# Kernel optimization log

Measured on AMD Instinct MI355X. Metric: run time of the kernel, lower is better.

Reference implementation:

```python
import jax, jax.numpy as jnp
import numpy as np
from jax import lax

L, B, T, C, F = 4, 4, 2048, 1024, 4096  # n_layer, batch, ctx_len, n_embd(=dim_att), dim_ffn
EPS = 1e-5


def setup_inputs() -> dict:
    key = jax.random.key(0)
    ks = jax.random.split(key, 16)
    s = 0.02
    d = {}
    d["x"] = jax.random.normal(ks[0], (B, T, C), jnp.float32)
    d["ln0_w"] = jnp.ones((C,), jnp.float32)
    d["ln0_b"] = jnp.zeros((C,), jnp.float32)
    d["ln1_w"] = jnp.ones((L, C), jnp.float32)
    d["ln1_b"] = jnp.zeros((L, C), jnp.float32)
    d["ln2_w"] = jnp.ones((L, C), jnp.float32)
    d["ln2_b"] = jnp.zeros((L, C), jnp.float32)
    d["time_decay"] = jax.random.normal(ks[1], (L, C), jnp.float32) * 0.5
    d["time_first"] = jax.random.normal(ks[2], (L, C), jnp.float32) * 0.5 + jnp.float32(np.log(0.3))
    d["tmk"] = jax.random.uniform(ks[3], (L, C), jnp.float32)
    d["tmv"] = jax.random.uniform(ks[4], (L, C), jnp.float32)
    d["tmr"] = jax.random.uniform(ks[5], (L, C), jnp.float32)
    d["Wk"] = jax.random.normal(ks[6], (L, C, C), jnp.float32) * s
    d["Wv"] = jax.random.normal(ks[7], (L, C, C), jnp.float32) * s
    d["Wr"] = jax.random.normal(ks[8], (L, C, C), jnp.float32) * s
    d["Wo"] = jax.random.normal(ks[9], (L, C, C), jnp.float32) * s
    d["cmk"] = jax.random.uniform(ks[10], (L, C), jnp.float32)
    d["cmr"] = jax.random.uniform(ks[11], (L, C), jnp.float32)
    d["Wck"] = jax.random.normal(ks[12], (L, F, C), jnp.float32) * s  # key: n_embd -> dim_ffn
    d["Wcv"] = jax.random.normal(ks[13], (L, C, F), jnp.float32) * s  # value: dim_ffn -> n_embd
    d["Wcr"] = jax.random.normal(ks[14], (L, C, C), jnp.float32) * s  # receptance
    return d


def layernorm(x, w, b):
    m = jnp.mean(x, axis=-1, keepdims=True)
    v = jnp.var(x, axis=-1, keepdims=True)
    return (x - m) * lax.rsqrt(v + EPS) * w + b


def time_shift(x):
    # ZeroPad2d((0,0,1,-1)): shift sequence right by one, zero at t=0
    return jnp.pad(x, ((0, 0), (1, 0), (0, 0)))[:, :-1]


def wkv(time_decay, time_first, k, v):
    # numerically-stable RWKV-4 WKV recurrence; k,v: [B,T,C]
    w = -jnp.exp(time_decay)  # [C]
    u = time_first            # [C]
    kt = jnp.swapaxes(k, 0, 1)  # [T,B,C]
    vt = jnp.swapaxes(v, 0, 1)
    Bn, Cn = k.shape[0], k.shape[2]
    init = (jnp.zeros((Bn, Cn), k.dtype), jnp.zeros((Bn, Cn), k.dtype),
            jnp.full((Bn, Cn), -1e38, k.dtype))

    def step(carry, kv):
        aa, bb, pp = carry
        kk, vv = kv
        ww = u + kk
        qq = jnp.maximum(pp, ww)
        e1 = jnp.exp(pp - qq)
        e2 = jnp.exp(ww - qq)
        out = (e1 * aa + e2 * vv) / (e1 * bb + e2)
        ww2 = pp + w
        qq2 = jnp.maximum(ww2, kk)
        e1b = jnp.exp(ww2 - qq2)
        e2b = jnp.exp(kk - qq2)
        return (e1b * aa + e2b * vv, e1b * bb + e2b, qq2), out

    _, out = lax.scan(step, init, (kt, vt))
    return jnp.swapaxes(out, 0, 1)  # [B,T,C]


def reference(x, ln0_w, ln0_b, ln1_w, ln1_b, ln2_w, ln2_b, time_decay, time_first,
              tmk, tmv, tmr, Wk, Wv, Wr, Wo, cmk, cmr, Wck, Wcv, Wcr):
    x = layernorm(x, ln0_w, ln0_b)  # ln0 on layer 0
    for l in range(L):
        # --- TimeMix ---
        h = layernorm(x, ln1_w[l], ln1_b[l])
        hh = time_shift(h)
        xk = h * tmk[l] + hh * (1 - tmk[l])
        xv = h * tmv[l] + hh * (1 - tmv[l])
        xr = h * tmr[l] + hh * (1 - tmr[l])
        k = jnp.einsum('btc,oc->bto', xk, Wk[l])
        v = jnp.einsum('btc,oc->bto', xv, Wv[l])
        sr = jax.nn.sigmoid(jnp.einsum('btc,oc->bto', xr, Wr[l]))
        rwkv = sr * wkv(time_decay[l], time_first[l], k, v)
        x = x + jnp.einsum('bto,co->btc', rwkv, Wo[l])
        # --- ChannelMix ---
        h = layernorm(x, ln2_w[l], ln2_b[l])
        hh = time_shift(h)
        xk = h * cmk[l] + hh * (1 - cmk[l])
        xr = h * cmr[l] + hh * (1 - cmr[l])
        kf = jnp.einsum('btc,fc->btf', xk, Wck[l])
        kf = jnp.square(jax.nn.relu(kf))
        kv = jnp.einsum('btf,cf->btc', kf, Wcv[l])
        x = x + jax.nn.sigmoid(jnp.einsum('btc,oc->bto', xr, Wcr[l])) * kv
    return x
```

## Files before the change

### kernel.cpp

```cpp
#include <hip/hip_runtime.h>
#include <cstdint>

#define TT 2048
#define CCH 1024
#define FFD 4096
#define EPSV 1e-5f
#define NCHK 32
#define CHKL 64

typedef __attribute__((ext_vector_type(4))) float floatx4;
typedef __attribute__((ext_vector_type(8))) short shortx8;

__device__ __forceinline__ unsigned short f32_to_bf16(float f){
  union { float f; unsigned int u; } x; x.f = f;
  unsigned int r = x.u + 0x7fffu + ((x.u >> 16) & 1u);
  return (unsigned short)(r >> 16);
}
__device__ __forceinline__ float bf16_to_f32(unsigned short h){
  union { unsigned int u; float f; } x; x.u = ((unsigned int)h) << 16;
  return x.f;
}
__device__ __forceinline__ float wave_sum(float v){
  #pragma unroll
  for (int o = 32; o > 0; o >>= 1) v += __shfl_down(v, o, 64);
  return v;
}
__device__ __forceinline__ void async16(const void* g, void* l){
  __builtin_amdgcn_global_load_lds((const __attribute__((address_space(1))) void*)g,
                                   (__attribute__((address_space(3))) void*)l, 16, 0, 0);
}

struct CvtArgs {
  const float* s[7];
  unsigned short* d[7];
  int n4[7];
};
__global__ __launch_bounds__(256) void cvt7_kernel(CvtArgs a){
  const int seg = blockIdx.y;
  const float* __restrict__ s = a.s[seg];
  unsigned short* __restrict__ d = a.d[seg];
  const int n4 = a.n4[seg];
  for (int i = blockIdx.x * 256 + threadIdx.x; i < n4; i += gridDim.x * 256) {
    float4 v = ((const float4*)s)[i];
    union { unsigned short u[4]; uint2 p; } o;
    o.u[0] = f32_to_bf16(v.x); o.u[1] = f32_to_bf16(v.y);
    o.u[2] = f32_to_bf16(v.z); o.u[3] = f32_to_bf16(v.w);
    *(uint2*)&d[(long)i * 4] = o.p;
  }
}

__global__ __launch_bounds__(256) void ln0_kernel(const float* __restrict__ xin,
    const float* __restrict__ w, const float* __restrict__ b, float* __restrict__ xo){
  const int row = blockIdx.x, tid = threadIdx.x;
  const float* xr = xin + (long)row * CCH;
  float c4[4]; float s = 0.f, s2 = 0.f;
  #pragma unroll
  for (int j = 0; j < 4; j++){ c4[j] = xr[tid + j*256]; s += c4[j]; s2 += c4[j]*c4[j]; }
  s = wave_sum(s); s2 = wave_sum(s2);
  __shared__ float red[2][4];
  const int wid = tid >> 6, lane = tid & 63;
  if (lane == 0){ red[0][wid] = s; red[1][wid] = s2; }
  __syncthreads();
  const float S  = red[0][0]+red[0][1]+red[0][2]+red[0][3];
  const float S2 = red[1][0]+red[1][1]+red[1][2]+red[1][3];
  const float inv = 1.f / CCH;
  const float m = S * inv;
  const float rs = rsqrtf(S2 * inv - m*m + EPSV);
  float* xout = xo + (long)row * CCH;
  #pragma unroll
  for (int j = 0; j < 4; j++){ int c = tid + j*256; xout[c] = (c4[j]-m)*rs*w[c] + b[c]; }
}

template<int NOUT>
__global__ __launch_bounds__(256) void ln_mix(
    const float* __restrict__ x,
    const float* __restrict__ lw, const float* __restrict__ lb,
    const float* __restrict__ mk, const float* __restrict__ mv, const float* __restrict__ mr,
    unsigned short* __restrict__ xk, unsigned short* __restrict__ xv, unsigned short* __restrict__ xr)
{
  const int row = blockIdx.x;
  const int t = row & (TT - 1);
  const int tid = threadIdx.x;
  const float* xc = x + (long)row * CCH;
  const float* xp = xc - CCH;
  float c4[4], p4[4];
  float s1=0.f, s2=0.f, s3=0.f, s4=0.f;
  #pragma unroll
  for (int j = 0; j < 4; j++){
    const int c = tid + j*256;
    c4[j] = xc[c];
    p4[j] = (t > 0) ? xp[c] : 0.f;
    s1 += c4[j]; s2 += c4[j]*c4[j];
    s3 += p4[j]; s4 += p4[j]*p4[j];
  }
  s1 = wave_sum(s1); s2 = wave_sum(s2); s3 = wave_sum(s3); s4 = wave_sum(s4);
  __shared__ float red[4][4];
  const int wid = tid >> 6, lane = tid & 63;
  if (lane == 0){ red[wid][0]=s1; red[wid][1]=s2; red[wid][2]=s3; red[wid][3]=s4; }
  __syncthreads();
  const float S1 = red[0][0]+red[1][0]+red[2][0]+red[3][0];
  const float S2 = red[0][1]+red[1][1]+red[2][1]+red[3][1];
  const float S3 = red[0][2]+red[1][2]+red[2][2]+red[3][2];
  const float S4 = red[0][3]+red[1][3]+red[2][3]+red[3][3];
  const float inv = 1.f / CCH;
  const float m1 = S1*inv; const float r1 = rsqrtf(S2*inv - m1*m1 + EPSV);
  const float m0 = S3*inv; const float r0 = rsqrtf(S4*inv - m0*m0 + EPSV);
  #pragma unroll
  for (int j = 0; j < 4; j++){
    const int c = tid + j*256;
    const long o = (long)row * CCH + c;
    const float wv = lw[c], bv = lb[c];
    const float h  = (c4[j]-m1)*r1*wv + bv;
    const float hp = (t > 0) ? ((p4[j]-m0)*r0*wv + bv) : 0.f;
    const float a = mk[c]; xk[o] = f32_to_bf16(h*a + hp*(1.f-a));
    if (NOUT == 3){ const float q = mv[c]; xv[o] = f32_to_bf16(h*q + hp*(1.f-q)); }
    const float g = mr[c]; xr[o] = f32_to_bf16(h*g + hp*(1.f-g));
  }
}

__global__ __launch_bounds__(256) void wkv_pass1(
    const unsigned short* __restrict__ kin, const unsigned short* __restrict__ vin,
    const float* __restrict__ td,
    float* __restrict__ sta, float* __restrict__ stb, float* __restrict__ stp)
{
  const int c = blockIdx.x * 256 + threadIdx.x;
  const int chunk = blockIdx.y, b = blockIdx.z;
  const float w = -__expf(td[c]);
  const long base = ((long)b * TT + (long)chunk * CHKL) * CCH + c;
  float aa = 0.f, bb = 0.f, pp = -1e38f;
  for (int t0 = 0; t0 < CHKL; t0 += 8) {
    float kr[8], vr[8];
    #pragma unroll
    for (int j = 0; j < 8; j++){
      const long o = base + (long)(t0 + j) * CCH;
      kr[j] = bf16_to_f32(kin[o]);
      vr[j] = bf16_to_f32(vin[o]);
    }
    #pragma unroll
    for (int j = 0; j < 8; j++){
      const float kk = kr[j], vv = vr[j];
      const float ww2 = pp + w;
      const float qq2 = fmaxf(ww2, kk);
      const float e1b = __expf(ww2 - qq2), e2b = __expf(kk - qq2);
      aa = e1b*aa + e2b*vv; bb = e1b*bb + e2b; pp = qq2;
    }
  }
  const long si = (long)chunk * 4096 + b * CCH + c;
  sta[si] = aa; stb[si] = bb; stp[si] = pp;
}

__global__ __launch_bounds__(256) void wkv_combine(
    const float* __restrict__ td,
    const float* __restrict__ sta, const float* __restrict__ stb, const float* __restrict__ stp,
    float* __restrict__ ina, float* __restrict__ inb, float* __restrict__ inp)
{
  const int idx = blockIdx.x * 256 + threadIdx.x;
  const int c = idx & (CCH - 1);
  const float wn = -__expf(td[c]) * (float)CHKL;
  float a = 0.f, b = 0.f, p = -1e38f;
  for (int j0 = 0; j0 < NCHK; j0 += 8) {
    float la[8], lb[8], lp[8];
    #pragma unroll
    for (int j = 0; j < 8; j++){
      const long si = (long)(j0 + j) * 4096 + idx;
      la[j] = sta[si]; lb[j] = stb[si]; lp[j] = stp[si];
    }
    #pragma unroll
    for (int j = 0; j < 8; j++){
      const long si = (long)(j0 + j) * 4096 + idx;
      ina[si] = a; inb[si] = b; inp[si] = p;
      const float pd = p + wn;
      const float q = fmaxf(pd, lp[j]);
      const float e1 = __expf(pd - q), e2 = __expf(lp[j] - q);
      a = e1*a + e2*la[j]; b = e1*b + e2*lb[j]; p = q;
    }
  }
}

__global__ __launch_bounds__(256) void wkv_pass2(
    const unsigned short* __restrict__ kin, const unsigned short* __restrict__ vin,
    const unsigned short* __restrict__ srin,
    const float* __restrict__ td, const float* __restrict__ tf,
    const float* __restrict__ ina, const float* __restrict__ inb, const float* __restrict__ inp,
    unsigned short* __restrict__ out)
{
  const int c = blockIdx.x * 256 + threadIdx.x;
  const int chunk = blockIdx.y, b = blockIdx.z;
  const float w = -__expf(td[c]);
  const float u = tf[c];
  const long si = (long)chunk * 4096 + b * CCH + c;
  float aa = ina[si], bb = inb[si], pp = inp[si];
  const long base = ((long)b * TT + (long)chunk * CHKL) * CCH + c;
  for (int t0 = 0; t0 < CHKL; t0 += 8) {
    float kr[8], vr[8], sr[8];
    #pragma unroll
    for (int j = 0; j < 8; j++){
      const long o = base + (long)(t0 + j) * CCH;
      kr[j] = bf16_to_f32(kin[o]);
      vr[j] = bf16_to_f32(vin[o]);
      sr[j] = bf16_to_f32(srin[o]);
    }
    #pragma unroll
    for (int j = 0; j < 8; j++){
      const float kk = kr[j], vv = vr[j];
      const float ww = u + kk;
      const float qq = fmaxf(pp, ww);
      const float e1 = __expf(pp - qq), e2 = __expf(ww - qq);
      const float outv = (e1*aa + e2*vv) / (e1*bb + e2);
      const float ww2 = pp + w;
      const float qq2 = fmaxf(ww2, kk);
      const float e1b = __expf(ww2 - qq2), e2b = __expf(kk - qq2);
      aa = e1b*aa + e2b*vv; bb = e1b*bb + e2b; pp = qq2;
      out[base + (long)(t0 + j) * CCH] = f32_to_bf16(sr[j] * outv);
    }
  }
}

#define BK 64

enum { EP_BF16 = 0, EP_ADD = 3, EP_MULADD = 4, EP_KVR = 5, EP_FFN1 = 6 };

template<int EPI, int BMt>
__global__ __launch_bounds__(256, 3) void gemm_bt(
    const unsigned short* __restrict__ A,
    const unsigned short* __restrict__ W,
    int N, const int K,
    unsigned short* __restrict__ outb,
    float* __restrict__ xres,
    const unsigned short* __restrict__ rr,
    const unsigned short* __restrict__ A2,
    const unsigned short* __restrict__ W2,
    unsigned short* __restrict__ outb2,
    const int N2)
{
  constexpr int MR = BMt / 2 / 16;
  constexpr int NR = 4;
  constexpr int AI = BMt / 32;

  const int bm = blockIdx.x;
  int bn = blockIdx.y;
  bool sig = false;
  if (EPI == EP_KVR) {
    const long z = blockIdx.z;
    const long Mfull = (long)gridDim.x * BMt;
    A    += z * Mfull * K;
    W    += z * (long)N * K;
    outb += z * Mfull * N;
    sig = (blockIdx.z == 2);
  }
  if (EPI == EP_FFN1) {
    if (blockIdx.z == 1) {
      if (bn >= N2 / 128) return;
      A = A2; W = W2; outb = outb2; N = N2; sig = true;
    }
  }
  __shared__ unsigned short lA[BMt * BK];
  __shared__ unsigned short lW[128 * BK];
  const int tid = threadIdx.x;
  const int wid = tid >> 6, lane = tid & 63;
  const int wm = (wid >> 1), wn = (wid & 1);
  const int quad = lane >> 4, r16 = lane & 15;

  const int srow = tid >> 3;
  const int scol = (tid & 7) ^ (srow & 7);
  const unsigned short* Ag = A + ((long)(bm * BMt + srow)) * K + scol * 8;
  const unsigned short* Wg = W + ((long)(bn * 128 + srow)) * K + scol * 8;
  const long rs32 = (long)32 * K;

  const int sw0 = ((quad)     ^ (r16 & 7)) * 8;
  const int sw1 = ((4 + quad) ^ (r16 & 7)) * 8;

  const floatx4 zf = {0.f, 0.f, 0.f, 0.f};
  floatx4 acc[MR][NR];
  #pragma unroll
  for (int i = 0; i < MR; i++)
    #pragma unroll
    for (int j = 0; j < NR; j++) acc[i][j] = zf;

  for (int k0 = 0; k0 < K; k0 += BK) {
    __syncthreads();
    #pragma unroll
    for (int i = 0; i < 4; i++) {
      if (BMt == 256) {
        async16(Ag + (long)(2*i)   * rs32 + k0, &lA[((2*i)   * 256 + tid) * 8]);
        async16(Ag + (long)(2*i+1) * rs32 + k0, &lA[((2*i+1) * 256 + tid) * 8]);
      } else {
        async16(Ag + (long)i * rs32 + k0, &lA[(i * 256 + tid) * 8]);
      }
      async16(Wg + (long)i * rs32 + k0, &lW[(i * 256 + tid) * 8]);
    }
    __syncthreads();
    #pragma unroll
    for (int kk = 0; kk < 2; kk++) {
      const int sw = kk ? sw1 : sw0;
      shortx8 af[MR], bf[NR];
      #pragma unroll
      for (int m = 0; m < MR; m++)
        af[m] = *(const shortx8*)&lA[(wm * (MR*16) + m*16 + r16) * 64 + sw];
      #pragma unroll
      for (int n = 0; n < NR; n++)
        bf[n] = *(const shortx8*)&lW[(wn * 64 + n*16 + r16) * 64 + sw];
      #pragma unroll
      for (int m = 0; m < MR; m++)
        #pragma unroll
        for (int n = 0; n < NR; n++)
          acc[m][n] = __builtin_amdgcn_mfma_f32_16x16x32_bf16(af[m], bf[n], acc[m][n], 0, 0, 0);
    }
  }

  const int colBase = bn * 128 + wn * 64 + r16;
  #pragma unroll
  for (int m = 0; m < MR; m++) {
    const int rowBase = bm * BMt + wm * (MR*16) + m * 16 + quad * 4;
    #pragma unroll
    for (int n = 0; n < NR; n++) {
      const int col = colBase + n * 16;
      #pragma unroll
      for (int r = 0; r < 4; r++) {
        const long idx = (long)(rowBase + r) * N + col;
        const float val = acc[m][n][r];
        if (EPI == EP_KVR)       outb[idx] = sig ? f32_to_bf16(1.f / (1.f + __expf(-val)))
                                                 : f32_to_bf16(val);
        else if (EPI == EP_FFN1) {
          if (sig) outb[idx] = f32_to_bf16(1.f / (1.f + __expf(-val)));
          else     { const float t = val > 0.f ? val : 0.f; outb[idx] = f32_to_bf16(t * t); }
        }
        else if (EPI == EP_ADD)  xres[idx] += val;
        else if (EPI == EP_MULADD) xres[idx] = fmaf(bf16_to_f32(rr[idx]), val, xres[idx]);
        else                     outb[idx] = f32_to_bf16(val);
      }
    }
  }
}

extern "C" void kernel_launch(void* const* d_in, const int* in_sizes, int n_in,
                              void* d_out, int out_size, void* d_ws, size_t ws_size,
                              hipStream_t stream)
{
  const float* x_in       = (const float*)d_in[0];
  const float* ln0_w      = (const float*)d_in[1];
  const float* ln0_b      = (const float*)d_in[2];
  const float* ln1_w      = (const float*)d_in[3];
  const float* ln1_b      = (const float*)d_in[4];
  const float* ln2_w      = (const float*)d_in[5];
  const float* ln2_b      = (const float*)d_in[6];
  const float* time_decay = (const float*)d_in[7];
  const float* time_first = (const float*)d_in[8];
  const float* tmk        = (const float*)d_in[9];
  const float* tmv        = (const float*)d_in[10];
  const float* tmr        = (const float*)d_in[11];
  const float* Wk         = (const float*)d_in[12];
  const float* Wv         = (const float*)d_in[13];
  const float* Wr         = (const float*)d_in[14];
  const float* Wo         = (const float*)d_in[15];
  const float* cmk        = (const float*)d_in[16];
  const float* cmr        = (const float*)d_in[17];
  const float* Wck        = (const float*)d_in[18];
  const float* Wcv        = (const float*)d_in[19];
  const float* Wcr        = (const float*)d_in[20];
  float* x = (float*)d_out;

  const int M = 4 * TT;
  const long lCC = (long)CCH * CCH;
  const long lFC = (long)FFD * CCH;
  const long MC  = (long)M * CCH;

  unsigned short* wsl  = (unsigned short*)d_ws;
  unsigned short* wkb  = wsl;
  unsigned short* wvb  = wkb + lCC;
  unsigned short* wrb  = wvb + lCC;
  unsigned short* wob  = wrb + lCC;
  unsigned short* wcrb = wob + lCC;
  unsigned short* wckb = wcrb + lCC;
  unsigned short* wcvb = wckb + lFC;
  unsigned short* xk   = wcvb + lFC;
  unsigned short* xv   = xk + MC;
  unsigned short* xr   = xv + MC;
  unsigned short* kbuf = xr + MC;
  unsigned short* vbuf = kbuf + MC;
  unsigned short* sbuf = vbuf + MC;
  unsigned short* kfb  = kbuf;
  unsigned short* rrb  = kbuf + (long)M * FFD;

  float* sta = (float*)xk;
  float* stb = sta + (long)NCHK * 4096;
  float* stp = stb + (long)NCHK * 4096;
  float* ina = stp + (long)NCHK * 4096;
  float* inb = ina + (long)NCHK * 4096;
  float* inp = inb + (long)NCHK * 4096;

  ln0_kernel<<<M, 256, 0, stream>>>(x_in, ln0_w, ln0_b, x);

  const dim3 gkvr(M / 256, CCH / 128, 3);
  const dim3 g1  (M / 128, CCH / 128);
  const dim3 gffn(M / 256, FFD / 128, 2);
  const dim3 gw(CCH / 256, NCHK, 4);

  for (int l = 0; l < 4; l++) {
    CvtArgs ca;
    ca.s[0] = Wk  + (long)l * lCC; ca.d[0] = wkb;  ca.n4[0] = (int)(lCC / 4);
    ca.s[1] = Wv  + (long)l * lCC; ca.d[1] = wvb;  ca.n4[1] = (int)(lCC / 4);
    ca.s[2] = Wr  + (long)l * lCC; ca.d[2] = wrb;  ca.n4[2] = (int)(lCC / 4);
    ca.s[3] = Wo  + (long)l * lCC; ca.d[3] = wob;  ca.n4[3] = (int)(lCC / 4);
    ca.s[4] = Wcr + (long)l * lCC; ca.d[4] = wcrb; ca.n4[4] = (int)(lCC / 4);
    ca.s[5] = Wck + (long)l * lFC; ca.d[5] = wckb; ca.n4[5] = (int)(lFC / 4);
    ca.s[6] = Wcv + (long)l * lFC; ca.d[6] = wcvb; ca.n4[6] = (int)(lFC / 4);
    cvt7_kernel<<<dim3(512, 7), 256, 0, stream>>>(ca);

    const float* td_l = time_decay + l*CCH;
    const float* tf_l = time_first + l*CCH;

    ln_mix<3><<<M, 256, 0, stream>>>(x, ln1_w + l*CCH, ln1_b + l*CCH,
                                     tmk + l*CCH, tmv + l*CCH, tmr + l*CCH, xk, xv, xr);
    gemm_bt<EP_KVR, 256><<<gkvr, 256, 0, stream>>>(xk, wkb, CCH, CCH, kbuf, nullptr,
                                              nullptr, nullptr, nullptr, nullptr, 0);
    wkv_pass1 <<<gw, 256, 0, stream>>>(kbuf, vbuf, td_l, sta, stb, stp);
    wkv_combine<<<16, 256, 0, stream>>>(td_l, sta, stb, stp, ina, inb, inp);
    wkv_pass2 <<<gw, 256, 0, stream>>>(kbuf, vbuf, sbuf, td_l, tf_l, ina, inb, inp, xv);
    gemm_bt<EP_ADD, 128><<<g1, 256, 0, stream>>>(xv, wob, CCH, CCH, nullptr, x, nullptr,
                                             nullptr, nullptr, nullptr, 0);

    ln_mix<2><<<M, 256, 0, stream>>>(x, ln2_w + l*CCH, ln2_b + l*CCH,
                                     cmk + l*CCH, nullptr, cmr + l*CCH, xk, nullptr, xr);
    gemm_bt<EP_FFN1, 256><<<gffn, 256, 0, stream>>>(xk, wckb, FFD, CCH, kfb, nullptr,
                                               nullptr, xr, wcrb, rrb, CCH);
    gemm_bt<EP_MULADD, 128><<<g1, 256, 0, stream>>>(kfb, wcvb, CCH, FFD, nullptr, x, rrb,
                                               nullptr, nullptr, nullptr, 0);
  }
}
```

Measured before the change: 1.622 ms.

## Triple-buffer GEMM LDS tiles with async prefetch and BK=32

Replaces the single-buffered BK=64 GEMM main loop, which had two barriers per k-step, with a three-stage LDS ring of BK=32 tiles. Global-to-LDS async loads run two steps ahead, guarded by explicit vmcnt waits and one barrier per step. MFMA sections are raised in priority with setprio, and the swizzle is adapted to the narrower tile. This is meant to hide global load latency behind MFMA work. In exchange it takes more LDS and lowers the occupancy hint from 3 to 2 blocks per CU.

```diff
diff --git a/kernel.cpp b/kernel.cpp
--- a/kernel.cpp
+++ b/kernel.cpp
@@ -216,12 +216,12 @@
   }
 }
 
-#define BK 64
+#define BK 32
 
 enum { EP_BF16 = 0, EP_ADD = 3, EP_MULADD = 4, EP_KVR = 5, EP_FFN1 = 6 };
 
 template<int EPI, int BMt>
-__global__ __launch_bounds__(256, 3) void gemm_bt(
+__global__ __launch_bounds__(256, 2) void gemm_bt(
     const unsigned short* __restrict__ A,
     const unsigned short* __restrict__ W,
     int N, const int K,
@@ -235,7 +235,9 @@
 {
   constexpr int MR = BMt / 2 / 16;
   constexpr int NR = 4;
-  constexpr int AI = BMt / 32;
+  constexpr int LA = BMt * 4 / 256;
+  constexpr int LB = 2;
+  constexpr int LPT = LA + LB;
 
   const int bm = blockIdx.x;
   int bn = blockIdx.y;
@@ -254,21 +256,34 @@
       A = A2; W = W2; outb = outb2; N = N2; sig = true;
     }
   }
-  __shared__ unsigned short lA[BMt * BK];
-  __shared__ unsigned short lW[128 * BK];
+  __shared__ unsigned short lA[3][BMt * BK];
+  __shared__ unsigned short lW[3][128 * BK];
   const int tid = threadIdx.x;
   const int wid = tid >> 6, lane = tid & 63;
   const int wm = (wid >> 1), wn = (wid & 1);
   const int quad = lane >> 4, r16 = lane & 15;
-
-  const int srow = tid >> 3;
-  const int scol = (tid & 7) ^ (srow & 7);
-  const unsigned short* Ag = A + ((long)(bm * BMt + srow)) * K + scol * 8;
-  const unsigned short* Wg = W + ((long)(bn * 128 + srow)) * K + scol * 8;
-  const long rs32 = (long)32 * K;
-
-  const int sw0 = ((quad)     ^ (r16 & 7)) * 8;
-  const int sw1 = ((4 + quad) ^ (r16 & 7)) * 8;
+  const int WR = wm * (MR * 16);
+
+  const unsigned short* aSrc[LA]; int aDst[LA];
+  #pragma unroll
+  for (int i = 0; i < LA; i++) {
+    const int P = i * 256 + tid;
+    const int row = P >> 2;
+    const int c = (P & 3) ^ (row & 3);
+    aSrc[i] = A + (long)(bm * BMt + row) * K + c * 8;
+    aDst[i] = P * 8;
+  }
+  const unsigned short* bSrc[LB]; int bDst[LB];
+  #pragma unroll
+  for (int i = 0; i < LB; i++) {
+    const int P = i * 256 + tid;
+    const int row = P >> 2;
+    const int c = (P & 3) ^ (row & 3);
+    bSrc[i] = W + (long)(bn * 128 + row) * K + c * 8;
+    bDst[i] = P * 8;
+  }
+
+  const int swq = (quad ^ (r16 & 3)) * 8;
 
   const floatx4 zf = {0.f, 0.f, 0.f, 0.f};
   floatx4 acc[MR][NR];
@@ -277,41 +292,59 @@
     #pragma unroll
     for (int j = 0; j < NR; j++) acc[i][j] = zf;
 
-  for (int k0 = 0; k0 < K; k0 += BK) {
-    __syncthreads();
-    #pragma unroll
-    for (int i = 0; i < 4; i++) {
-      if (BMt == 256) {
-        async16(Ag + (long)(2*i)   * rs32 + k0, &lA[((2*i)   * 256 + tid) * 8]);
-        async16(Ag + (long)(2*i+1) * rs32 + k0, &lA[((2*i+1) * 256 + tid) * 8]);
-      } else {
-        async16(Ag + (long)i * rs32 + k0, &lA[(i * 256 + tid) * 8]);
-      }
-      async16(Wg + (long)i * rs32 + k0, &lW[(i * 256 + tid) * 8]);
-    }
-    __syncthreads();
-    #pragma unroll
-    for (int kk = 0; kk < 2; kk++) {
-      const int sw = kk ? sw1 : sw0;
-      shortx8 af[MR], bf[NR];
+  const int NT = K / BK;
+
+  #pragma unroll
+  for (int tt = 0; tt < 2; ++tt) {
+    const long ko = (long)tt * BK;
+    #pragma unroll
+    for (int i = 0; i < LA; i++) async16(aSrc[i] + ko, &lA[tt][aDst[i]]);
+    #pragma unroll
+    for (int i = 0; i < LB; i++) async16(bSrc[i] + ko, &lW[tt][bDst[i]]);
+  }
+  asm volatile("s_waitcnt vmcnt(%0)" :: "n"(LPT) : "memory");
+  __builtin_amdgcn_s_barrier();
+  __builtin_amdgcn_sched_barrier(0);
+
+  int s = 0, s2 = 2;
+  for (int t = 0; t < NT; ++t) {
+    if (t + 2 < NT) {
+      const long ko = (long)(t + 2) * BK;
       #pragma unroll
-      for (int m = 0; m < MR; m++)
-        af[m] = *(const shortx8*)&lA[(wm * (MR*16) + m*16 + r16) * 64 + sw];
+      for (int i = 0; i < LA; i++) async16(aSrc[i] + ko, &lA[s2][aDst[i]]);
+      #pragma unroll
+      for (int i = 0; i < LB; i++) async16(bSrc[i] + ko, &lW[s2][bDst[i]]);
+    }
+    shortx8 af[MR], bf[NR];
+    #pragma unroll
+    for (int m = 0; m < MR; m++)
+      af[m] = *(const shortx8*)&lA[s][(WR + m * 16 + r16) * BK + swq];
+    #pragma unroll
+    for (int n = 0; n < NR; n++)
+      bf[n] = *(const shortx8*)&lW[s][(wn * 64 + n * 16 + r16) * BK + swq];
+    __builtin_amdgcn_s_setprio(1);
+    #pragma unroll
+    for (int m = 0; m < MR; m++)
       #pragma unroll
       for (int n = 0; n < NR; n++)
-        bf[n] = *(const shortx8*)&lW[(wn * 64 + n*16 + r16) * 64 + sw];
-      #pragma unroll
-      for (int m = 0; m < MR; m++)
-        #pragma unroll
-        for (int n = 0; n < NR; n++)
-          acc[m][n] = __builtin_amdgcn_mfma_f32_16x16x32_bf16(af[m], bf[n], acc[m][n], 0, 0, 0);
-    }
+        acc[m][n] = __builtin_amdgcn_mfma_f32_16x16x32_bf16(af[m], bf[n], acc[m][n], 0, 0, 0);
+    __builtin_amdgcn_s_setprio(0);
+    __builtin_amdgcn_sched_barrier(0);
+    if (t + 2 < NT)      asm volatile("s_waitcnt vmcnt(%0)" :: "n"(LPT) : "memory");
+    else if (t + 1 < NT) asm volatile("s_waitcnt vmcnt(0)" ::: "memory");
+    if (t + 1 < NT) {
+      asm volatile("s_waitcnt lgkmcnt(0)" ::: "memory");
+      __builtin_amdgcn_s_barrier();
+      __builtin_amdgcn_sched_barrier(0);
+    }
+    s = (s == 2) ? 0 : s + 1;
+    s2 = (s2 == 2) ? 0 : s2 + 1;
   }
 
   const int colBase = bn * 128 + wn * 64 + r16;
   #pragma unroll
   for (int m = 0; m < MR; m++) {
-    const int rowBase = bm * BMt + wm * (MR*16) + m * 16 + quad * 4;
+    const int rowBase = bm * BMt + WR + m * 16 + quad * 4;
     #pragma unroll
     for (int n = 0; n < NR; n++) {
       const int col = colBase + n * 16;
```

Result: slower. 1.923 ms (+18.6%).

## Fuse weight conversion into ln_mix, inline WKV combine, add double-buffered GEMM

Applied to the files above, without the earlier changes.

The bf16 weight conversion now runs as extra grid rows of the first ln_mix launch, which removes one kernel launch per layer. The chunk-state combine kernel is removed: each pass2 block recomputes its prefix state serially over the earlier chunks, trading redundant work for one fewer launch and less buffer traffic. A new 128x128 double-buffered GEMM with async LDS loads and occupancy of two handles the output and FFN value projections. The risks are a slower GEMM and load imbalance from the prefix loop in later chunks.

```diff
diff --git a/kernel.cpp b/kernel.cpp
--- a/kernel.cpp
+++ b/kernel.cpp
@@ -35,8 +35,7 @@
   unsigned short* d[7];
   int n4[7];
 };
-__global__ __launch_bounds__(256) void cvt7_kernel(CvtArgs a){
-  const int seg = blockIdx.y;
+__device__ __forceinline__ void cvt_body(const CvtArgs& a, int seg){
   const float* __restrict__ s = a.s[seg];
   unsigned short* __restrict__ d = a.d[seg];
   const int n4 = a.n4[seg];
@@ -72,7 +71,7 @@
 }
 
 template<int NOUT>
-__global__ __launch_bounds__(256) void ln_mix(
+__device__ __forceinline__ void lnmix_body(
     const float* __restrict__ x,
     const float* __restrict__ lw, const float* __restrict__ lb,
     const float* __restrict__ mk, const float* __restrict__ mv, const float* __restrict__ mr,
@@ -118,6 +117,29 @@
   }
 }
 
+template<int NOUT>
+__global__ __launch_bounds__(256) void ln_mix(
+    const float* __restrict__ x,
+    const float* __restrict__ lw, const float* __restrict__ lb,
+    const float* __restrict__ mk, const float* __restrict__ mv, const float* __restrict__ mr,
+    unsigned short* __restrict__ xk, unsigned short* __restrict__ xv, unsigned short* __restrict__ xr)
+{
+  lnmix_body<NOUT>(x, lw, lb, mk, mv, mr, xk, xv, xr);
+}
+
+__global__ __launch_bounds__(256) void lnmix3_cvt(CvtArgs a,
+    const float* __restrict__ x,
+    const float* __restrict__ lw, const float* __restrict__ lb,
+    const float* __restrict__ mk, const float* __restrict__ mv, const float* __restrict__ mr,
+    unsigned short* __restrict__ xk, unsigned short* __restrict__ xv, unsigned short* __restrict__ xr)
+{
+  if (blockIdx.y == 0) {
+    lnmix_body<3>(x, lw, lb, mk, mv, mr, xk, xv, xr);
+  } else {
+    cvt_body(a, blockIdx.y - 1);
+  }
+}
+
 __global__ __launch_bounds__(256) void wkv_pass1(
     const unsigned short* __restrict__ kin, const unsigned short* __restrict__ vin,
     const float* __restrict__ td,
@@ -149,47 +171,27 @@
   sta[si] = aa; stb[si] = bb; stp[si] = pp;
 }
 
-__global__ __launch_bounds__(256) void wkv_combine(
-    const float* __restrict__ td,
-    const float* __restrict__ sta, const float* __restrict__ stb, const float* __restrict__ stp,
-    float* __restrict__ ina, float* __restrict__ inb, float* __restrict__ inp)
-{
-  const int idx = blockIdx.x * 256 + threadIdx.x;
-  const int c = idx & (CCH - 1);
-  const float wn = -__expf(td[c]) * (float)CHKL;
-  float a = 0.f, b = 0.f, p = -1e38f;
-  for (int j0 = 0; j0 < NCHK; j0 += 8) {
-    float la[8], lb[8], lp[8];
-    #pragma unroll
-    for (int j = 0; j < 8; j++){
-      const long si = (long)(j0 + j) * 4096 + idx;
-      la[j] = sta[si]; lb[j] = stb[si]; lp[j] = stp[si];
-    }
-    #pragma unroll
-    for (int j = 0; j < 8; j++){
-      const long si = (long)(j0 + j) * 4096 + idx;
-      ina[si] = a; inb[si] = b; inp[si] = p;
-      const float pd = p + wn;
-      const float q = fmaxf(pd, lp[j]);
-      const float e1 = __expf(pd - q), e2 = __expf(lp[j] - q);
-      a = e1*a + e2*la[j]; b = e1*b + e2*lb[j]; p = q;
-    }
-  }
-}
-
 __global__ __launch_bounds__(256) void wkv_pass2(
     const unsigned short* __restrict__ kin, const unsigned short* __restrict__ vin,
     const unsigned short* __restrict__ srin,
     const float* __restrict__ td, const float* __restrict__ tf,
-    const float* __restrict__ ina, const float* __restrict__ inb, const float* __restrict__ inp,
+    const float* __restrict__ sta, const float* __restrict__ stb, const float* __restrict__ stp,
     unsigned short* __restrict__ out)
 {
   const int c = blockIdx.x * 256 + threadIdx.x;
   const int chunk = blockIdx.y, b = blockIdx.z;
   const float w = -__expf(td[c]);
   const float u = tf[c];
-  const long si = (long)chunk * 4096 + b * CCH + c;
-  float aa = ina[si], bb = inb[si], pp = inp[si];
+  const float wn = w * (float)CHKL;
+  float aa = 0.f, bb = 0.f, pp = -1e38f;
+  for (int j = 0; j < chunk; ++j) {
+    const long sj = (long)j * 4096 + b * CCH + c;
+    const float la = sta[sj], lb = stb[sj], lp = stp[sj];
+    const float pd = pp + wn;
+    const float q = fmaxf(pd, lp);
+    const float e1 = __expf(pd - q), e2 = __expf(lp - q);
+    aa = e1*aa + e2*la; bb = e1*bb + e2*lb; pp = q;
+  }
   const long base = ((long)b * TT + (long)chunk * CHKL) * CCH + c;
   for (int t0 = 0; t0 < CHKL; t0 += 8) {
     float kr[8], vr[8], sr[8];
@@ -235,7 +237,6 @@
 {
   constexpr int MR = BMt / 2 / 16;
   constexpr int NR = 4;
-  constexpr int AI = BMt / 32;
 
   const int bm = blockIdx.x;
   int bn = blockIdx.y;
@@ -328,6 +329,103 @@
         else if (EPI == EP_ADD)  xres[idx] += val;
         else if (EPI == EP_MULADD) xres[idx] = fmaf(bf16_to_f32(rr[idx]), val, xres[idx]);
         else                     outb[idx] = f32_to_bf16(val);
+      }
+    }
+  }
+}
+
+template<int EPI>
+__global__ __launch_bounds__(256, 2) void gemm2p(
+    const unsigned short* __restrict__ A,
+    const unsigned short* __restrict__ W,
+    const int N, const int K,
+    float* __restrict__ xres,
+    const unsigned short* __restrict__ rr)
+{
+  __shared__ unsigned short lA[2][128 * BK];
+  __shared__ unsigned short lW[2][128 * BK];
+  const int bm = blockIdx.x, bn = blockIdx.y;
+  const int tid = threadIdx.x;
+  const int wid = tid >> 6, lane = tid & 63;
+  const int wm = (wid >> 1), wn = (wid & 1);
+  const int quad = lane >> 4, r16 = lane & 15;
+
+  const int srow = tid >> 3;
+  const int scol = (tid & 7) ^ (srow & 7);
+  const unsigned short* Ag = A + ((long)(bm * 128 + srow)) * K + scol * 8;
+  const unsigned short* Wg = W + ((long)(bn * 128 + srow)) * K + scol * 8;
+  const long rs32 = (long)32 * K;
+
+  const int sw0 = ((quad)     ^ (r16 & 7)) * 8;
+  const int sw1 = ((4 + quad) ^ (r16 & 7)) * 8;
+
+  const floatx4 zf = {0.f, 0.f, 0.f, 0.f};
+  floatx4 acc[4][4];
+  #pragma unroll
+  for (int i = 0; i < 4; i++)
+    #pragma unroll
+    for (int j = 0; j < 4; j++) acc[i][j] = zf;
+
+  const int NT = K / BK;
+
+  #pragma unroll
+  for (int i = 0; i < 4; i++) {
+    async16(Ag + (long)i * rs32, &lA[0][(i * 256 + tid) * 8]);
+    async16(Wg + (long)i * rs32, &lW[0][(i * 256 + tid) * 8]);
+  }
+  asm volatile("s_waitcnt vmcnt(0)" ::: "memory");
+  __builtin_amdgcn_s_barrier();
+  __builtin_amdgcn_sched_barrier(0);
+
+  int cur = 0;
+  for (int t = 0; t < NT; ++t) {
+    if (t + 1 < NT) {
+      const long k0 = (long)(t + 1) * BK;
+      const int nb = cur ^ 1;
+      #pragma unroll
+      for (int i = 0; i < 4; i++) {
+        async16(Ag + (long)i * rs32 + k0, &lA[nb][(i * 256 + tid) * 8]);
+        async16(Wg + (long)i * rs32 + k0, &lW[nb][(i * 256 + tid) * 8]);
+      }
+    }
+    __builtin_amdgcn_sched_barrier(0);
+    #pragma unroll
+    for (int kk = 0; kk < 2; kk++) {
+      const int sw = kk ? sw1 : sw0;
+      shortx8 af[4], bf[4];
+      #pragma unroll
+      for (int m = 0; m < 4; m++) af[m] = *(const shortx8*)&lA[cur][(wm * 64 + m*16 + r16) * 64 + sw];
+      #pragma unroll
+      for (int n = 0; n < 4; n++) bf[n] = *(const shortx8*)&lW[cur][(wn * 64 + n*16 + r16) * 64 + sw];
+      __builtin_amdgcn_s_setprio(1);
+      #pragma unroll
+      for (int m = 0; m < 4; m++)
+        #pragma unroll
+        for (int n = 0; n < 4; n++)
+          acc[m][n] = __builtin_amdgcn_mfma_f32_16x16x32_bf16(af[m], bf[n], acc[m][n], 0, 0, 0);
+      __builtin_amdgcn_s_setprio(0);
+    }
+    if (t + 1 < NT) {
+      asm volatile("s_waitcnt vmcnt(0)" ::: "memory");
+      __builtin_amdgcn_s_barrier();
+      __builtin_amdgcn_sched_barrier(0);
+      cur ^= 1;
+    }
+  }
+
+  const int colBase = bn * 128 + wn * 64 + r16;
+  #pragma unroll
+  for (int m = 0; m < 4; m++) {
+    const int rowBase = bm * 128 + wm * 64 + m * 16 + quad * 4;
+    #pragma unroll
+    for (int n = 0; n < 4; n++) {
+      const int col = colBase + n * 16;
+      #pragma unroll
+      for (int r = 0; r < 4; r++) {
+        const long idx = (long)(rowBase + r) * N + col;
+        const float val = acc[m][n][r];
+        if (EPI == EP_ADD)       xres[idx] += val;
+        else if (EPI == EP_MULADD) xres[idx] = fmaf(bf16_to_f32(rr[idx]), val, xres[idx]);
       }
     }
   }
@@ -385,9 +483,6 @@
   float* sta = (float*)xk;
   float* stb = sta + (long)NCHK * 4096;
   float* stp = stb + (long)NCHK * 4096;
-  float* ina = stp + (long)NCHK * 4096;
-  float* inb = ina + (long)NCHK * 4096;
-  float* inp = inb + (long)NCHK * 4096;
 
   ln0_kernel<<<M, 256, 0, stream>>>(x_in, ln0_w, ln0_b, x);
 
@@ -395,6 +490,7 @@
   const dim3 g1  (M / 128, CCH / 128);
   const dim3 gffn(M / 256, FFD / 128, 2);
   const dim3 gw(CCH / 256, NCHK, 4);
+  const dim3 gfuse(M, 8);
 
   for (int l = 0; l < 4; l++) {
     CvtArgs ca;
@@ -405,26 +501,22 @@
     ca.s[4] = Wcr + (long)l * lCC; ca.d[4] = wcrb; ca.n4[4] = (int)(lCC / 4);
     ca.s[5] = Wck + (long)l * lFC; ca.d[5] = wckb; ca.n4[5] = (int)(lFC / 4);
     ca.s[6] = Wcv + (long)l * lFC; ca.d[6] = wcvb; ca.n4[6] = (int)(lFC / 4);
-    cvt7_kernel<<<dim3(512, 7), 256, 0, stream>>>(ca);
 
     const float* td_l = time_decay + l*CCH;
     const float* tf_l = time_first + l*CCH;
 
-    ln_mix<3><<<M, 256, 0, stream>>>(x, ln1_w + l*CCH, ln1_b + l*CCH,
-                                     tmk + l*CCH, tmv + l*CCH, tmr + l*CCH, xk, xv, xr);
+    lnmix3_cvt<<<gfuse, 256, 0, stream>>>(ca, x, ln1_w + l*CCH, ln1_b + l*CCH,
+                                          tmk + l*CCH, tmv + l*CCH, tmr + l*CCH, xk, xv, xr);
     gemm_bt<EP_KVR, 256><<<gkvr, 256, 0, stream>>>(xk, wkb, CCH, CCH, kbuf, nullptr,
                                               nullptr, nullptr, nullptr, nullptr, 0);
     wkv_pass1 <<<gw, 256, 0, stream>>>(kbuf, vbuf, td_l, sta, stb, stp);
-    wkv_combine<<<16, 256, 0, stream>>>(td_l, sta, stb, stp, ina, inb, inp);
-    wkv_pass2 <<<gw, 256, 0, stream>>>(kbuf, vbuf, sbuf, td_l, tf_l, ina, inb, inp, xv);
-    gemm_bt<EP_ADD, 128><<<g1, 256, 0, stream>>>(xv, wob, CCH, CCH, nullptr, x, nullptr,
-                                             nullptr, nullptr, nullptr, 0);
+    wkv_pass2 <<<gw, 256, 0, stream>>>(kbuf, vbuf, sbuf, td_l, tf_l, sta, stb, stp, xv);
+    gemm2p<EP_ADD><<<g1, 256, 0, stream>>>(xv, wob, CCH, CCH, x, nullptr);
 
     ln_mix<2><<<M, 256, 0, stream>>>(x, ln2_w + l*CCH, ln2_b + l*CCH,
                                      cmk + l*CCH, nullptr, cmr + l*CCH, xk, nullptr, xr);
     gemm_bt<EP_FFN1, 256><<<gffn, 256, 0, stream>>>(xk, wckb, FFD, CCH, kfb, nullptr,
                                                nullptr, xr, wcrb, rrb, CCH);
-    gemm_bt<EP_MULADD, 128><<<g1, 256, 0, stream>>>(kfb, wcvb, CCH, FFD, nullptr, x, rrb,
-                                               nullptr, nullptr, nullptr, 0);
-  }
-}
+    gemm2p<EP_MULADD><<<g1, 256, 0, stream>>>(kfb, wcvb, CCH, FFD, x, rrb);
+  }
+}
```

Result: no change. 1.611 ms (-0.7%).
